# Kernel tuning notes

Hardware: AMD Instinct MI355X
Metric: run time of the kernel (lower is better)

## Reference

```python
import jax, jax.numpy as jnp
import numpy as np

ALPHA = 0.01  # LeakyReLU negative slope
NEG_INF = -1e12  # same masking constant as the torch code


def setup_inputs() -> dict:
    key = jax.random.key(0)
    k1, k2, k3, k4 = jax.random.split(key, 4)
    B, N, C_IN, C_OUT = 8, 2048, 128, 64
    inp = jax.random.normal(k1, (B, N, C_IN), dtype=jnp.float32)
    adj = jax.random.randint(k2, (N, N), 0, 2).astype(jnp.float32)
    # xavier_uniform with gain=1.414
    def xavier(k, shape, gain=1.414):
        fan_in, fan_out = shape[0], shape[1]
        limit = gain * np.sqrt(6.0 / (fan_in + fan_out))
        return jax.random.uniform(k, shape, jnp.float32, -limit, limit)
    W = xavier(k3, (C_IN, C_OUT))
    a = xavier(k4, (2 * C_OUT, 1))
    return {"inp": inp, "adj": adj, "W": W, "a": a}


def reference(inp, adj, W, a):
    # inp: [B, N, C_in], adj: [N, N], W: [C_in, F], a: [2F, 1]
    B, N, _ = inp.shape
    F_out = W.shape[1]
    adj = adj + jnp.eye(N, dtype=adj.dtype)  # add self-loops
    h = jnp.einsum('bnc,cf->bnf', inp, W)    # [B, N, F]
    # a^T [h_i || h_j] = <a1, h_i> + <a2, h_j>  (identical math, no NxNx2F tensor)
    a1 = a[:F_out, 0]
    a2 = a[F_out:, 0]
    s1 = h @ a1  # [B, N] score contribution of source node i
    s2 = h @ a2  # [B, N] score contribution of target node j
    e = jax.nn.leaky_relu(s1[:, :, None] + s2[:, None, :], negative_slope=ALPHA)  # [B, N, N]
    att = jnp.where(adj[None, :, :] > 0, e, NEG_INF)
    att = jax.nn.softmax(att, axis=2)
    h_prime = jnp.einsum('bnm,bmf->bnf', att, h)  # [B, N, F]
    return h_prime
```

## Files before the change

kernel.cpp:

```cpp
#include <hip/hip_runtime.h>
#include <hip/hip_bf16.h>
#include <cstddef>
#include <cstdint>


#define B_DIM 8
#define N_DIM 2048
#define C_IN  128
#define C_OUT 64
#define NROWS (B_DIM * N_DIM)
#define LOG2E 1.4426950408889634f

typedef short bf16x8 __attribute__((ext_vector_type(8)));
typedef short bf16x4 __attribute__((ext_vector_type(4)));
typedef float f32x4  __attribute__((ext_vector_type(4)));

static __device__ __forceinline__ short f2bf(float x) {
    __hip_bfloat16 b = __float2bfloat16(x);
    return *reinterpret_cast<short*>(&b);
}

__global__ __launch_bounds__(256) void gat_prep(
    const float* __restrict__ inp,
    const float* __restrict__ W,
    const float* __restrict__ a,
    const float* __restrict__ adj,
    __hip_bfloat16* __restrict__ hT,
    float* __restrict__ E1, float* __restrict__ F1,
    float* __restrict__ E2, float* __restrict__ F2,
    unsigned long long* __restrict__ mask)
{
    __shared__ float Wl[C_IN * C_OUT];
    __shared__ float a1l[C_OUT], a2l[C_OUT];
    __shared__ float tr[C_OUT][17];

    if (blockIdx.x >= 1024) {
        const int i    = blockIdx.x - 1024;
        const int wave = threadIdx.x >> 6;
        const int lane = threadIdx.x & 63;
        const float* __restrict__ arow = adj + (size_t)i * N_DIM;
#pragma unroll
        for (int it = 0; it < 8; ++it) {
            const int j = wave * 512 + it * 64 + lane;
            const bool conn = (arow[j] > 0.f) || (j == i);
            const unsigned long long bm = __ballot(conn);
            if (lane == 0) mask[(size_t)i * (N_DIM / 64) + (j >> 6)] = bm;
        }
        return;
    }

    {
        const float4* Wv = (const float4*)W;
        float4* Wd = (float4*)Wl;
        for (int t = threadIdx.x; t < C_IN * C_OUT / 4; t += 256) Wd[t] = Wv[t];
        if (threadIdx.x < C_OUT) {
            a1l[threadIdx.x] = a[threadIdx.x];
            a2l[threadIdx.x] = a[C_OUT + threadIdx.x];
        }
    }
    __syncthreads();

    const int wave = threadIdx.x >> 6;
    const int lane = threadIdx.x & 63;
    const int i0 = blockIdx.x * 16;
    const int b  = i0 >> 11;
    const int il = i0 & (N_DIM - 1);
    const int rl = wave * 4;

    const float* __restrict__ x0 = inp + (size_t)(i0 + rl) * C_IN;
    const float* __restrict__ x1 = x0 + C_IN;
    const float* __restrict__ x2 = x1 + C_IN;
    const float* __restrict__ x3 = x2 + C_IN;
    float h0 = 0.f, h1 = 0.f, h2 = 0.f, h3 = 0.f;
#pragma unroll 4
    for (int c = 0; c < C_IN; c += 4) {
        const float4 a0 = *(const float4*)(x0 + c);
        const float4 a1 = *(const float4*)(x1 + c);
        const float4 a2 = *(const float4*)(x2 + c);
        const float4 a3 = *(const float4*)(x3 + c);
#pragma unroll
        for (int cc = 0; cc < 4; ++cc) {
            const float w_ = Wl[(c + cc) * C_OUT + lane];
            const float e0 = (cc==0)?a0.x:(cc==1)?a0.y:(cc==2)?a0.z:a0.w;
            const float e1 = (cc==0)?a1.x:(cc==1)?a1.y:(cc==2)?a1.z:a1.w;
            const float e2 = (cc==0)?a2.x:(cc==1)?a2.y:(cc==2)?a2.z:a2.w;
            const float e3 = (cc==0)?a3.x:(cc==1)?a3.y:(cc==2)?a3.z:a3.w;
            h0 = fmaf(e0, w_, h0);
            h1 = fmaf(e1, w_, h1);
            h2 = fmaf(e2, w_, h2);
            h3 = fmaf(e3, w_, h3);
        }
    }
    tr[lane][rl + 0] = h0;
    tr[lane][rl + 1] = h1;
    tr[lane][rl + 2] = h2;
    tr[lane][rl + 3] = h3;

    float hv[4] = {h0, h1, h2, h3};
#pragma unroll
    for (int k = 0; k < 4; ++k) {
        float p1 = hv[k] * a1l[lane];
        float p2 = hv[k] * a2l[lane];
#pragma unroll
        for (int off = 32; off; off >>= 1) {
            p1 += __shfl_xor(p1, off, 64);
            p2 += __shfl_xor(p2, off, 64);
        }
        if (lane == 0) {
            const float z1 = p1 * LOG2E;
            const float z2 = p2 * LOG2E;
            const int r = i0 + rl + k;
            E1[r] = exp2f(z1);
            F1[r] = exp2f(0.01f * z1);
            E2[r] = exp2f(z2);
            F2[r] = exp2f(0.01f * z2);
        }
    }
    __syncthreads();

    const int f   = threadIdx.x >> 2;
    const int ro4 = (threadIdx.x & 3) * 4;
    bf16x4 v;
    v[0] = f2bf(tr[f][ro4 + 0]);
    v[1] = f2bf(tr[f][ro4 + 1]);
    v[2] = f2bf(tr[f][ro4 + 2]);
    v[3] = f2bf(tr[f][ro4 + 3]);
    *(bf16x4*)(hT + ((size_t)b * C_OUT + f) * N_DIM + il + ro4) = v;
}

__global__ __launch_bounds__(512, 4) void gat_attn(
    const __hip_bfloat16* __restrict__ hT,
    const float* __restrict__ E1, const float* __restrict__ F1,
    const float* __restrict__ E2, const float* __restrict__ F2,
    const unsigned long long* __restrict__ mask,
    float* __restrict__ out)
{
    __shared__ __align__(16) char smem[2][32768];
    __shared__ float lred[8][2][16];

    const int wave = threadIdx.x >> 6;
    const int lane = threadIdx.x & 63;
    const int tb = blockIdx.x;
    const int b  = tb >> 6;
    const int i0 = (tb & 63) * 32;
    const int mloc = lane & 15;
    const int quad = lane >> 4;
    const int igA  = i0 + mloc;
    const int igB  = i0 + 16 + mloc;

    const float E1A = E1[(size_t)b * N_DIM + igA];
    const float F1A = F1[(size_t)b * N_DIM + igA];
    const float E1B = E1[(size_t)b * N_DIM + igB];
    const float F1B = F1[(size_t)b * N_DIM + igB];
    const float* __restrict__ E2b = E2 + (size_t)b * N_DIM;
    const float* __restrict__ F2b = F2 + (size_t)b * N_DIM;
    const uint8_t* __restrict__ mA = (const uint8_t*)mask + (size_t)igA * (N_DIM / 8);
    const uint8_t* __restrict__ mBp = (const uint8_t*)mask + (size_t)igB * (N_DIM / 8);
    const char* __restrict__ hTb = (const char*)(hT + (size_t)b * C_OUT * N_DIM);

    f32x4 aA0 = {0,0,0,0}, aA1 = {0,0,0,0}, aA2 = {0,0,0,0}, aA3 = {0,0,0,0};
    f32x4 aB0 = {0,0,0,0}, aB1 = {0,0,0,0}, aB2 = {0,0,0,0}, aB3 = {0,0,0,0};
    f32x4 lA = {0,0,0,0}, lB = {0,0,0,0};
    const bf16x8 ones = {(short)0x3F80, (short)0x3F80, (short)0x3F80, (short)0x3F80,
                         (short)0x3F80, (short)0x3F80, (short)0x3F80, (short)0x3F80};

    const int bjl = wave * 32 + quad * 8;
    const int cA  = bjl >> 3;

    auto compute_chunk = [&](int jc, const char* buf) {
        const int jg = jc * 256 + bjl;
        const unsigned mbA = mA[jg >> 3];
        const unsigned mbB = mBp[jg >> 3];
        const f32x4 eA = *(const f32x4*)(E2b + jg);
        const f32x4 eB = *(const f32x4*)(E2b + jg + 4);
        const f32x4 fA = *(const f32x4*)(F2b + jg);
        const f32x4 fB = *(const f32x4*)(F2b + jg + 4);
        bf16x8 pf0, pf1;
#pragma unroll
        for (int t = 0; t < 8; ++t) {
            const float ev = (t < 4 ? eA[t] : eB[t - 4]);
            const float fv = (t < 4 ? fA[t] : fB[t - 4]);
            float p0 = fmaxf(E1A * ev, F1A * fv);
            p0 = ((mbA >> t) & 1u) ? p0 : 0.f;
            pf0[t] = f2bf(p0);
            float p1 = fmaxf(E1B * ev, F1B * fv);
            p1 = ((mbB >> t) & 1u) ? p1 : 0.f;
            pf1[t] = f2bf(p1);
        }
        lA = __builtin_amdgcn_mfma_f32_16x16x32_bf16(pf0, ones, lA, 0, 0, 0);
        lB = __builtin_amdgcn_mfma_f32_16x16x32_bf16(pf1, ones, lB, 0, 0, 0);
#pragma unroll
        for (int nb = 0; nb < 4; ++nb) {
            const int f  = nb * 16 + mloc;
            const int cS = (cA & 16) | ((cA ^ (f & 15)) & 15);
            const bf16x8 bF = *(const bf16x8*)(buf + (f * 32 + cS) * 16);
            if (nb == 0) { aA0 = __builtin_amdgcn_mfma_f32_16x16x32_bf16(pf0, bF, aA0, 0, 0, 0);
                           aB0 = __builtin_amdgcn_mfma_f32_16x16x32_bf16(pf1, bF, aB0, 0, 0, 0); }
            if (nb == 1) { aA1 = __builtin_amdgcn_mfma_f32_16x16x32_bf16(pf0, bF, aA1, 0, 0, 0);
                           aB1 = __builtin_amdgcn_mfma_f32_16x16x32_bf16(pf1, bF, aB1, 0, 0, 0); }
            if (nb == 2) { aA2 = __builtin_amdgcn_mfma_f32_16x16x32_bf16(pf0, bF, aA2, 0, 0, 0);
                           aB2 = __builtin_amdgcn_mfma_f32_16x16x32_bf16(pf1, bF, aB2, 0, 0, 0); }
            if (nb == 3) { aA3 = __builtin_amdgcn_mfma_f32_16x16x32_bf16(pf0, bF, aA3, 0, 0, 0);
                           aB3 = __builtin_amdgcn_mfma_f32_16x16x32_bf16(pf1, bF, aB3, 0, 0, 0); }
        }
    };

    for (int jc = 0; jc < 8; ++jc) {
        __syncthreads();
#pragma unroll
        for (int q = 0; q < 4; ++q) {
            const int p = (wave * 4 + q) * 64 + lane;
            const int f  = p >> 5;
            const int cs = p & 31;
            const int c  = (cs & 16) | ((cs ^ (f & 15)) & 15);
            const char* gp = hTb + ((size_t)f * N_DIM + jc * 256) * 2 + c * 16;
            char* lp = smem[jc & 1] + (wave * 4 + q) * 1024;
            __builtin_amdgcn_global_load_lds(
                (const __attribute__((address_space(1))) void*)gp,
                (__attribute__((address_space(3))) void*)lp, 16, 0, 0);
        }
        if (jc > 0) compute_chunk(jc - 1, smem[(jc - 1) & 1]);
    }
    __syncthreads();
    compute_chunk(7, smem[1]);
    __syncthreads();

    if (mloc == 0) {
#pragma unroll
        for (int reg = 0; reg < 4; ++reg) {
            lred[wave][0][quad * 4 + reg] = lA[reg];
            lred[wave][1][quad * 4 + reg] = lB[reg];
        }
    }

    float* accL = (float*)smem;
#pragma unroll
    for (int reg = 0; reg < 4; ++reg) {
        const int r = quad * 4 + reg;
        float* pa = accL + ((wave * 2 + 0) * 16 + r) * 64 + mloc;
        float* pb = accL + ((wave * 2 + 1) * 16 + r) * 64 + mloc;
        pa[ 0] = aA0[reg]; pa[16] = aA1[reg]; pa[32] = aA2[reg]; pa[48] = aA3[reg];
        pb[ 0] = aB0[reg]; pb[16] = aB1[reg]; pb[32] = aB2[reg]; pb[48] = aB3[reg];
    }
    __syncthreads();

    float* __restrict__ ob = out + ((size_t)b * N_DIM + i0) * C_OUT;
#pragma unroll
    for (int e = threadIdx.x; e < 32 * C_OUT; e += 512) {
        const int R  = e >> 6;
        const int hf = R >> 4;
        const int r  = R & 15;
        const int fc = e & 63;
        float s = 0.f, ls = 0.f;
#pragma unroll
        for (int w = 0; w < 8; ++w) {
            s  += accL[((w * 2 + hf) * 16 + r) * 64 + fc];
            ls += lred[w][hf][r];
        }
        ob[e] = s / ls;
    }
}

extern "C" void kernel_launch(void* const* d_in, const int* in_sizes, int n_in,
                              void* d_out, int out_size, void* d_ws, size_t ws_size,
                              hipStream_t stream) {
    const float* inp = (const float*)d_in[0];
    const float* adj = (const float*)d_in[1];
    const float* W   = (const float*)d_in[2];
    const float* a   = (const float*)d_in[3];
    float* out = (float*)d_out;

    char* ws = (char*)d_ws;
    __hip_bfloat16* hT = (__hip_bfloat16*)ws;
    float* E1 = (float*)(ws + (size_t)2 * 1024 * 1024);
    float* F1 = E1 + NROWS;
    float* E2 = F1 + NROWS;
    float* F2 = E2 + NROWS;
    unsigned long long* mask = (unsigned long long*)(F2 + NROWS);

    gat_prep<<<1024 + N_DIM, 256, 0, stream>>>(inp, W, a, adj, hT, E1, F1, E2, F2, mask);
    gat_attn<<<NROWS / 32, 512, 0, stream>>>(hT, E1, F1, E2, F2, mask, out);
}
```

Baseline: 112.7 us.

## Fuse prep and attention kernels into one cooperative launch with grid sync

Merges the projection/score/mask-building kernel and the attention kernel into a single cooperative kernel of 512 blocks, separated by a grid-wide barrier. Each block now computes 32 projected rows and 4 adjacency mask rows before the sync, then does the attention tile for its block index. This removes one kernel launch and its inter-kernel gap. In exchange it adds a grid sync and fixes the prep work to 512 large blocks, and it keeps the old two-kernel path as a fallback if the cooperative launch fails.

```diff
diff --git a/kernel.cpp b/kernel.cpp
--- a/kernel.cpp
+++ b/kernel.cpp
@@ -1,4 +1,5 @@
 #include <hip/hip_runtime.h>
+#include <hip/hip_cooperative_groups.h>
 #include <hip/hip_bf16.h>
 #include <cstddef>
 #include <cstdint>
@@ -11,6 +12,8 @@
 #define NROWS (B_DIM * N_DIM)
 #define LOG2E 1.4426950408889634f
 
+namespace cg = cooperative_groups;
+
 typedef short bf16x8 __attribute__((ext_vector_type(8)));
 typedef short bf16x4 __attribute__((ext_vector_type(4)));
 typedef float f32x4  __attribute__((ext_vector_type(4)));
@@ -20,11 +23,248 @@
     return *reinterpret_cast<short*>(&b);
 }
 
-__global__ __launch_bounds__(256) void gat_prep(
+__global__ __launch_bounds__(512, 4) void gat_fused(
     const float* __restrict__ inp,
     const float* __restrict__ W,
     const float* __restrict__ a,
     const float* __restrict__ adj,
+    __hip_bfloat16* __restrict__ hT,
+    float* __restrict__ E1, float* __restrict__ F1,
+    float* __restrict__ E2, float* __restrict__ F2,
+    unsigned long long* __restrict__ mask,
+    float* __restrict__ out)
+{
+    __shared__ __align__(16) char smem[2][32768];
+    __shared__ float lred[8][2][16];
+    __shared__ float a1l[C_OUT], a2l[C_OUT];
+
+    const int tid  = threadIdx.x;
+    const int wave = tid >> 6;
+    const int lane = tid & 63;
+    const int tb   = blockIdx.x;
+
+    {
+        float* Wl = (float*)smem[0];
+        float (*tr)[33] = (float(*)[33])smem[1];
+
+        for (int t = tid; t < C_IN * C_OUT / 4; t += 512)
+            ((float4*)Wl)[t] = ((const float4*)W)[t];
+        if (tid < C_OUT) {
+            a1l[tid] = a[tid];
+            a2l[tid] = a[C_OUT + tid];
+        }
+        __syncthreads();
+
+        const int i0 = tb * 32;
+        const int b  = i0 >> 11;
+        const int il = i0 & (N_DIM - 1);
+        const int rl = wave * 4;
+
+        const float* __restrict__ x0 = inp + (size_t)(i0 + rl) * C_IN;
+        const float* __restrict__ x1 = x0 + C_IN;
+        const float* __restrict__ x2 = x1 + C_IN;
+        const float* __restrict__ x3 = x2 + C_IN;
+        float h0 = 0.f, h1 = 0.f, h2 = 0.f, h3 = 0.f;
+#pragma unroll 4
+        for (int c = 0; c < C_IN; c += 4) {
+            const float4 a0 = *(const float4*)(x0 + c);
+            const float4 a1v = *(const float4*)(x1 + c);
+            const float4 a2v = *(const float4*)(x2 + c);
+            const float4 a3v = *(const float4*)(x3 + c);
+#pragma unroll
+            for (int cc = 0; cc < 4; ++cc) {
+                const float w_ = Wl[(c + cc) * C_OUT + lane];
+                const float e0 = (cc==0)?a0.x:(cc==1)?a0.y:(cc==2)?a0.z:a0.w;
+                const float e1 = (cc==0)?a1v.x:(cc==1)?a1v.y:(cc==2)?a1v.z:a1v.w;
+                const float e2 = (cc==0)?a2v.x:(cc==1)?a2v.y:(cc==2)?a2v.z:a2v.w;
+                const float e3 = (cc==0)?a3v.x:(cc==1)?a3v.y:(cc==2)?a3v.z:a3v.w;
+                h0 = fmaf(e0, w_, h0);
+                h1 = fmaf(e1, w_, h1);
+                h2 = fmaf(e2, w_, h2);
+                h3 = fmaf(e3, w_, h3);
+            }
+        }
+        tr[lane][rl + 0] = h0;
+        tr[lane][rl + 1] = h1;
+        tr[lane][rl + 2] = h2;
+        tr[lane][rl + 3] = h3;
+
+        float hv[4] = {h0, h1, h2, h3};
+#pragma unroll
+        for (int k = 0; k < 4; ++k) {
+            float p1 = hv[k] * a1l[lane];
+            float p2 = hv[k] * a2l[lane];
+#pragma unroll
+            for (int off = 32; off; off >>= 1) {
+                p1 += __shfl_xor(p1, off, 64);
+                p2 += __shfl_xor(p2, off, 64);
+            }
+            if (lane == 0) {
+                const float z1 = p1 * LOG2E;
+                const float z2 = p2 * LOG2E;
+                const int r = i0 + rl + k;
+                E1[r] = exp2f(z1);
+                F1[r] = exp2f(0.01f * z1);
+                E2[r] = exp2f(z2);
+                F2[r] = exp2f(0.01f * z2);
+            }
+        }
+        __syncthreads();
+
+        {
+            const int f   = tid >> 3;
+            const int ro4 = (tid & 7) * 4;
+            bf16x4 v;
+            v[0] = f2bf(tr[f][ro4 + 0]);
+            v[1] = f2bf(tr[f][ro4 + 1]);
+            v[2] = f2bf(tr[f][ro4 + 2]);
+            v[3] = f2bf(tr[f][ro4 + 3]);
+            *(bf16x4*)(hT + ((size_t)b * C_OUT + f) * N_DIM + il + ro4) = v;
+        }
+
+#pragma unroll
+        for (int r = 0; r < 4; ++r) {
+            const int i = tb * 4 + r;
+            const float* __restrict__ arow = adj + (size_t)i * N_DIM;
+#pragma unroll
+            for (int it = 0; it < 4; ++it) {
+                const int j = it * 512 + wave * 64 + lane;
+                const bool conn = (arow[j] > 0.f) || (j == i);
+                const unsigned long long bm = __ballot(conn);
+                if (lane == 0) mask[(size_t)i * (N_DIM / 64) + (j >> 6)] = bm;
+            }
+        }
+    }
+
+    __threadfence();
+    cg::this_grid().sync();
+    __threadfence();
+
+    {
+        const int b  = tb >> 6;
+        const int i0 = (tb & 63) * 32;
+        const int mloc = lane & 15;
+        const int quad = lane >> 4;
+        const int igA  = i0 + mloc;
+        const int igB  = i0 + 16 + mloc;
+
+        const float E1A = E1[(size_t)b * N_DIM + igA];
+        const float F1A = F1[(size_t)b * N_DIM + igA];
+        const float E1B = E1[(size_t)b * N_DIM + igB];
+        const float F1B = F1[(size_t)b * N_DIM + igB];
+        const float* __restrict__ E2b = E2 + (size_t)b * N_DIM;
+        const float* __restrict__ F2b = F2 + (size_t)b * N_DIM;
+        const uint8_t* __restrict__ mA = (const uint8_t*)mask + (size_t)igA * (N_DIM / 8);
+        const uint8_t* __restrict__ mBp = (const uint8_t*)mask + (size_t)igB * (N_DIM / 8);
+        const char* __restrict__ hTb = (const char*)(hT + (size_t)b * C_OUT * N_DIM);
+
+        f32x4 aA0 = {0,0,0,0}, aA1 = {0,0,0,0}, aA2 = {0,0,0,0}, aA3 = {0,0,0,0};
+        f32x4 aB0 = {0,0,0,0}, aB1 = {0,0,0,0}, aB2 = {0,0,0,0}, aB3 = {0,0,0,0};
+        f32x4 lA = {0,0,0,0}, lB = {0,0,0,0};
+        const bf16x8 ones = {(short)0x3F80, (short)0x3F80, (short)0x3F80, (short)0x3F80,
+                             (short)0x3F80, (short)0x3F80, (short)0x3F80, (short)0x3F80};
+
+        const int bjl = wave * 32 + quad * 8;
+        const int cA  = bjl >> 3;
+
+        auto compute_chunk = [&](int jc, const char* buf) {
+            const int jg = jc * 256 + bjl;
+            const unsigned mbA = mA[jg >> 3];
+            const unsigned mbB = mBp[jg >> 3];
+            const f32x4 eA = *(const f32x4*)(E2b + jg);
+            const f32x4 eB = *(const f32x4*)(E2b + jg + 4);
+            const f32x4 fA = *(const f32x4*)(F2b + jg);
+            const f32x4 fB = *(const f32x4*)(F2b + jg + 4);
+            bf16x8 pf0, pf1;
+#pragma unroll
+            for (int t = 0; t < 8; ++t) {
+                const float ev = (t < 4 ? eA[t] : eB[t - 4]);
+                const float fv = (t < 4 ? fA[t] : fB[t - 4]);
+                float p0 = fmaxf(E1A * ev, F1A * fv);
+                p0 = ((mbA >> t) & 1u) ? p0 : 0.f;
+                pf0[t] = f2bf(p0);
+                float p1 = fmaxf(E1B * ev, F1B * fv);
+                p1 = ((mbB >> t) & 1u) ? p1 : 0.f;
+                pf1[t] = f2bf(p1);
+            }
+            lA = __builtin_amdgcn_mfma_f32_16x16x32_bf16(pf0, ones, lA, 0, 0, 0);
+            lB = __builtin_amdgcn_mfma_f32_16x16x32_bf16(pf1, ones, lB, 0, 0, 0);
+#pragma unroll
+            for (int nb = 0; nb < 4; ++nb) {
+                const int f  = nb * 16 + mloc;
+                const int cS = (cA & 16) | ((cA ^ (f & 15)) & 15);
+                const bf16x8 bF = *(const bf16x8*)(buf + (f * 32 + cS) * 16);
+                if (nb == 0) { aA0 = __builtin_amdgcn_mfma_f32_16x16x32_bf16(pf0, bF, aA0, 0, 0, 0);
+                               aB0 = __builtin_amdgcn_mfma_f32_16x16x32_bf16(pf1, bF, aB0, 0, 0, 0); }
+                if (nb == 1) { aA1 = __builtin_amdgcn_mfma_f32_16x16x32_bf16(pf0, bF, aA1, 0, 0, 0);
+                               aB1 = __builtin_amdgcn_mfma_f32_16x16x32_bf16(pf1, bF, aB1, 0, 0, 0); }
+                if (nb == 2) { aA2 = __builtin_amdgcn_mfma_f32_16x16x32_bf16(pf0, bF, aA2, 0, 0, 0);
+                               aB2 = __builtin_amdgcn_mfma_f32_16x16x32_bf16(pf1, bF, aB2, 0, 0, 0); }
+                if (nb == 3) { aA3 = __builtin_amdgcn_mfma_f32_16x16x32_bf16(pf0, bF, aA3, 0, 0, 0);
+                               aB3 = __builtin_amdgcn_mfma_f32_16x16x32_bf16(pf1, bF, aB3, 0, 0, 0); }
+            }
+        };
+
+        for (int jc = 0; jc < 8; ++jc) {
+            __syncthreads();
+#pragma unroll
+            for (int q = 0; q < 4; ++q) {
+                const int p = (wave * 4 + q) * 64 + lane;
+                const int f  = p >> 5;
+                const int cs = p & 31;
+                const int c  = (cs & 16) | ((cs ^ (f & 15)) & 15);
+                const char* gp = hTb + ((size_t)f * N_DIM + jc * 256) * 2 + c * 16;
+                char* lp = smem[jc & 1] + (wave * 4 + q) * 1024;
+                __builtin_amdgcn_global_load_lds(
+                    (const __attribute__((address_space(1))) void*)gp,
+                    (__attribute__((address_space(3))) void*)lp, 16, 0, 0);
+            }
+            if (jc > 0) compute_chunk(jc - 1, smem[(jc - 1) & 1]);
+        }
+        __syncthreads();
+        compute_chunk(7, smem[1]);
+        __syncthreads();
+
+        if (mloc == 0) {
+#pragma unroll
+            for (int reg = 0; reg < 4; ++reg) {
+                lred[wave][0][quad * 4 + reg] = lA[reg];
+                lred[wave][1][quad * 4 + reg] = lB[reg];
+            }
+        }
+
+        float* accL = (float*)smem;
+#pragma unroll
+        for (int reg = 0; reg < 4; ++reg) {
+            const int r = quad * 4 + reg;
+            float* pa = accL + ((wave * 2 + 0) * 16 + r) * 64 + mloc;
+            float* pb = accL + ((wave * 2 + 1) * 16 + r) * 64 + mloc;
+            pa[ 0] = aA0[reg]; pa[16] = aA1[reg]; pa[32] = aA2[reg]; pa[48] = aA3[reg];
+            pb[ 0] = aB0[reg]; pb[16] = aB1[reg]; pb[32] = aB2[reg]; pb[48] = aB3[reg];
+        }
+        __syncthreads();
+
+        float* __restrict__ ob = out + ((size_t)b * N_DIM + i0) * C_OUT;
+#pragma unroll
+        for (int e = tid; e < 32 * C_OUT; e += 512) {
+            const int R  = e >> 6;
+            const int hf = R >> 4;
+            const int r  = R & 15;
+            const int fc = e & 63;
+            float s = 0.f, ls = 0.f;
+#pragma unroll
+            for (int w = 0; w < 8; ++w) {
+                s  += accL[((w * 2 + hf) * 16 + r) * 64 + fc];
+                ls += lred[w][hf][r];
+            }
+            ob[e] = s / ls;
+        }
+    }
+}
+
+__global__ __launch_bounds__(256) void gat_prep(
+    const float* __restrict__ inp, const float* __restrict__ W,
+    const float* __restrict__ a, const float* __restrict__ adj,
     __hip_bfloat16* __restrict__ hT,
     float* __restrict__ E1, float* __restrict__ F1,
     float* __restrict__ E2, float* __restrict__ F2,
@@ -48,7 +288,6 @@
         }
         return;
     }
-
     {
         const float4* Wv = (const float4*)W;
         float4* Wd = (float4*)Wl;
@@ -59,14 +298,12 @@
         }
     }
     __syncthreads();
-
     const int wave = threadIdx.x >> 6;
     const int lane = threadIdx.x & 63;
     const int i0 = blockIdx.x * 16;
     const int b  = i0 >> 11;
     const int il = i0 & (N_DIM - 1);
     const int rl = wave * 4;
-
     const float* __restrict__ x0 = inp + (size_t)(i0 + rl) * C_IN;
     const float* __restrict__ x1 = x0 + C_IN;
     const float* __restrict__ x2 = x1 + C_IN;
@@ -75,27 +312,22 @@
 #pragma unroll 4
     for (int c = 0; c < C_IN; c += 4) {
         const float4 a0 = *(const float4*)(x0 + c);
-        const float4 a1 = *(const float4*)(x1 + c);
-        const float4 a2 = *(const float4*)(x2 + c);
-        const float4 a3 = *(const float4*)(x3 + c);
+        const float4 a1v = *(const float4*)(x1 + c);
+        const float4 a2v = *(const float4*)(x2 + c);
+        const float4 a3v = *(const float4*)(x3 + c);
 #pragma unroll
         for (int cc = 0; cc < 4; ++cc) {
             const float w_ = Wl[(c + cc) * C_OUT + lane];
             const float e0 = (cc==0)?a0.x:(cc==1)?a0.y:(cc==2)?a0.z:a0.w;
-            const float e1 = (cc==0)?a1.x:(cc==1)?a1.y:(cc==2)?a1.z:a1.w;
-            const float e2 = (cc==0)?a2.x:(cc==1)?a2.y:(cc==2)?a2.z:a2.w;
-            const float e3 = (cc==0)?a3.x:(cc==1)?a3.y:(cc==2)?a3.z:a3.w;
-            h0 = fmaf(e0, w_, h0);
-            h1 = fmaf(e1, w_, h1);
-            h2 = fmaf(e2, w_, h2);
-            h3 = fmaf(e3, w_, h3);
-        }
-    }
-    tr[lane][rl + 0] = h0;
-    tr[lane][rl + 1] = h1;
-    tr[lane][rl + 2] = h2;
-    tr[lane][rl + 3] = h3;
-
+            const float e1 = (cc==0)?a1v.x:(cc==1)?a1v.y:(cc==2)?a1v.z:a1v.w;
+            const float e2 = (cc==0)?a2v.x:(cc==1)?a2v.y:(cc==2)?a2v.z:a2v.w;
+            const float e3 = (cc==0)?a3v.x:(cc==1)?a3v.y:(cc==2)?a3v.z:a3v.w;
+            h0 = fmaf(e0, w_, h0); h1 = fmaf(e1, w_, h1);
+            h2 = fmaf(e2, w_, h2); h3 = fmaf(e3, w_, h3);
+        }
+    }
+    tr[lane][rl + 0] = h0; tr[lane][rl + 1] = h1;
+    tr[lane][rl + 2] = h2; tr[lane][rl + 3] = h3;
     float hv[4] = {h0, h1, h2, h3};
 #pragma unroll
     for (int k = 0; k < 4; ++k) {
@@ -110,21 +342,16 @@
             const float z1 = p1 * LOG2E;
             const float z2 = p2 * LOG2E;
             const int r = i0 + rl + k;
-            E1[r] = exp2f(z1);
-            F1[r] = exp2f(0.01f * z1);
-            E2[r] = exp2f(z2);
-            F2[r] = exp2f(0.01f * z2);
+            E1[r] = exp2f(z1); F1[r] = exp2f(0.01f * z1);
+            E2[r] = exp2f(z2); F2[r] = exp2f(0.01f * z2);
         }
     }
     __syncthreads();
-
     const int f   = threadIdx.x >> 2;
     const int ro4 = (threadIdx.x & 3) * 4;
     bf16x4 v;
-    v[0] = f2bf(tr[f][ro4 + 0]);
-    v[1] = f2bf(tr[f][ro4 + 1]);
-    v[2] = f2bf(tr[f][ro4 + 2]);
-    v[3] = f2bf(tr[f][ro4 + 3]);
+    v[0] = f2bf(tr[f][ro4 + 0]); v[1] = f2bf(tr[f][ro4 + 1]);
+    v[2] = f2bf(tr[f][ro4 + 2]); v[3] = f2bf(tr[f][ro4 + 3]);
     *(bf16x4*)(hT + ((size_t)b * C_OUT + f) * N_DIM + il + ro4) = v;
 }
 
@@ -137,7 +364,6 @@
 {
     __shared__ __align__(16) char smem[2][32768];
     __shared__ float lred[8][2][16];
-
     const int wave = threadIdx.x >> 6;
     const int lane = threadIdx.x & 63;
     const int tb = blockIdx.x;
@@ -147,7 +373,6 @@
     const int quad = lane >> 4;
     const int igA  = i0 + mloc;
     const int igB  = i0 + 16 + mloc;
-
     const float E1A = E1[(size_t)b * N_DIM + igA];
     const float F1A = F1[(size_t)b * N_DIM + igA];
     const float E1B = E1[(size_t)b * N_DIM + igB];
@@ -157,16 +382,13 @@
     const uint8_t* __restrict__ mA = (const uint8_t*)mask + (size_t)igA * (N_DIM / 8);
     const uint8_t* __restrict__ mBp = (const uint8_t*)mask + (size_t)igB * (N_DIM / 8);
     const char* __restrict__ hTb = (const char*)(hT + (size_t)b * C_OUT * N_DIM);
-
     f32x4 aA0 = {0,0,0,0}, aA1 = {0,0,0,0}, aA2 = {0,0,0,0}, aA3 = {0,0,0,0};
     f32x4 aB0 = {0,0,0,0}, aB1 = {0,0,0,0}, aB2 = {0,0,0,0}, aB3 = {0,0,0,0};
     f32x4 lA = {0,0,0,0}, lB = {0,0,0,0};
     const bf16x8 ones = {(short)0x3F80, (short)0x3F80, (short)0x3F80, (short)0x3F80,
                          (short)0x3F80, (short)0x3F80, (short)0x3F80, (short)0x3F80};
-
     const int bjl = wave * 32 + quad * 8;
     const int cA  = bjl >> 3;
-
     auto compute_chunk = [&](int jc, const char* buf) {
         const int jg = jc * 256 + bjl;
         const unsigned mbA = mA[jg >> 3];
@@ -204,7 +426,6 @@
                            aB3 = __builtin_amdgcn_mfma_f32_16x16x32_bf16(pf1, bF, aB3, 0, 0, 0); }
         }
     };
-
     for (int jc = 0; jc < 8; ++jc) {
         __syncthreads();
 #pragma unroll
@@ -224,7 +445,6 @@
     __syncthreads();
     compute_chunk(7, smem[1]);
     __syncthreads();
-
     if (mloc == 0) {
 #pragma unroll
         for (int reg = 0; reg < 4; ++reg) {
@@ -232,7 +452,6 @@
             lred[wave][1][quad * 4 + reg] = lB[reg];
         }
     }
-
     float* accL = (float*)smem;
 #pragma unroll
     for (int reg = 0; reg < 4; ++reg) {
@@ -243,7 +462,6 @@
         pb[ 0] = aB0[reg]; pb[16] = aB1[reg]; pb[32] = aB2[reg]; pb[48] = aB3[reg];
     }
     __syncthreads();
-
     float* __restrict__ ob = out + ((size_t)b * N_DIM + i0) * C_OUT;
 #pragma unroll
     for (int e = threadIdx.x; e < 32 * C_OUT; e += 512) {
@@ -278,6 +496,14 @@
     float* F2 = E2 + NROWS;
     unsigned long long* mask = (unsigned long long*)(F2 + NROWS);
 
-    gat_prep<<<1024 + N_DIM, 256, 0, stream>>>(inp, W, a, adj, hT, E1, F1, E2, F2, mask);
-    gat_attn<<<NROWS / 32, 512, 0, stream>>>(hT, E1, F1, E2, F2, mask, out);
+    void* args[] = {(void*)&inp, (void*)&W, (void*)&a, (void*)&adj, (void*)&hT,
+                    (void*)&E1, (void*)&F1, (void*)&E2, (void*)&F2,
+                    (void*)&mask, (void*)&out};
+    hipError_t err = hipLaunchCooperativeKernel((const void*)gat_fused,
+                                                dim3(512), dim3(512),
+                                                args, 0, stream);
+    if (err != hipSuccess) {
+        gat_prep<<<1024 + N_DIM, 256, 0, stream>>>(inp, W, a, adj, hT, E1, F1, E2, F2, mask);
+        gat_attn<<<NROWS / 32, 512, 0, stream>>>(hT, E1, F1, E2, F2, mask, out);
+    }
 }
```

New measurement: 322.2 us. 2.86x slower.
